# Performance work log

Hardware: AMD Instinct MI355X
Metric: run time of the kernel (lower is better)

The kernel has to match this reference:

```python
import jax, jax.numpy as jnp
import numpy as np

N = 50000      # nodes
E = 800000     # edges (avg degree 16)
F_IN = 128
H = 128


def setup_inputs() -> dict:
    key = jax.random.key(0)
    k = jax.random.split(key, 6)
    x = jax.random.normal(k[0], (N, F_IN), dtype=jnp.float32)
    edge_index = jax.random.randint(k[1], (2, E), 0, N, dtype=jnp.int64)
    perm = jax.random.permutation(k[2], N).astype(jnp.int64)
    # GCNConv params (PyG default: weight [F_in,H] applied as x @ W, bias [H])
    W = jax.random.normal(k[3], (F_IN, H), dtype=jnp.float32) / np.sqrt(F_IN)
    b = jnp.zeros((H,), dtype=jnp.float32)
    # nn.Bilinear(H, H, 1): weight [1,H,H], bias [1]
    bound = 1.0 / np.sqrt(H)
    Wb = jax.random.uniform(k[4], (1, H, H), dtype=jnp.float32, minval=-bound, maxval=bound)
    bb = jax.random.uniform(k[5], (1,), dtype=jnp.float32, minval=-bound, maxval=bound)
    return {"x": x, "W": W, "b": b, "Wb": Wb, "bb": bb,
            "edge_index": edge_index, "perm": perm}


def _gcn_conv(x, W, b, edge_index):
    # GCNConv: D^{-1/2} (A + I) D^{-1/2} X W + b  (symmetric norm, self-loops)
    xw = x @ W                               # [N, H] dense transform first
    loops = jnp.arange(N, dtype=edge_index.dtype)
    src = jnp.concatenate([edge_index[0], loops])   # [E+N]
    dst = jnp.concatenate([edge_index[1], loops])
    deg = jax.ops.segment_sum(jnp.ones_like(dst, dtype=xw.dtype), dst,
                              num_segments=N)        # in-degree incl. self-loop
    dinv = jnp.where(deg > 0, jax.lax.rsqrt(deg), 0.0)
    coef = dinv[src] * dinv[dst]                     # [E+N]
    msg = xw[src] * coef[:, None]                    # gather + scale
    z = jax.ops.segment_sum(msg, dst, num_segments=N) + b
    return z


def _bilinear(z1, z2, Wb, bb):
    # nn.Bilinear with out_features=1: score_n = z1_n^T Wb[0] z2_n + bb
    return jnp.einsum('nh,hg,ng->n', z1, Wb[0], z2)[:, None] + bb


def reference(x, W, b, Wb, bb, edge_index, perm):
    z = _gcn_conv(x, W, b, edge_index)
    positive_score = _bilinear(z, z, Wb, bb)
    negative_score = _bilinear(z, z[perm], Wb, bb)
    return (positive_score, negative_score)
```

## Files before the change

kernel.cpp:

```cpp
#include <hip/hip_runtime.h>
#include <hip/hip_bf16.h>

#define NN 50000
#define NE 800000
#define HD 128
#define WPAD 136

#define BINSH 9
#define NBINS 98
#define BINCAP 9216
#define CHUNK 1024
#define MAXBIN 9216

#define GEMM_BLOCKS ((NN + 63) / 64)
#define BIN_BLOCKS  ((NE + CHUNK - 1) / CHUNK)

typedef __attribute__((ext_vector_type(8))) short bf16x8;
typedef __attribute__((ext_vector_type(4))) float f32x4;

__device__ inline unsigned short f2bf(float f) {
    union { float f; unsigned u; } c; c.f = f;
    unsigned r = c.u + 0x7fff + ((c.u >> 16) & 1);
    return (unsigned short)(r >> 16);
}

__device__ inline float bflo(unsigned u) { return __uint_as_float(u << 16); }
__device__ inline float b2f(unsigned short u) { return __uint_as_float(((unsigned)u) << 16); }
__device__ inline float bfhi(unsigned u) { return __uint_as_float(u & 0xffff0000u); }

__device__ inline void split2(float v, unsigned short* h, unsigned short* l) {
    unsigned short hh = f2bf(v);
    float fh = __uint_as_float(((unsigned)hh) << 16);
    *h = hh;
    *l = f2bf(v - fh);
}

__device__ inline float4 ld_bf4(const unsigned short* p) {
    uint2 q = *(const uint2*)p;
    float4 r;
    r.x = bflo(q.x); r.y = bfhi(q.x);
    r.z = bflo(q.y); r.w = bfhi(q.y);
    return r;
}

__global__ __launch_bounds__(256) void k_prep(
        const float* __restrict__ W, const float* __restrict__ Wb, int* cursor,
        unsigned short* __restrict__ Wtg,
        unsigned short* __restrict__ Wbth, unsigned short* __restrict__ Wbtl) {
    int t = threadIdx.x;
    if (blockIdx.x == 0 && t < NBINS) cursor[t] = t * BINCAP;
    int idx = blockIdx.x * 256 + t;
    if (idx < HD * HD) {
        int h = idx >> 7, c = idx & 127;
        Wtg[c * WPAD + h] = f2bf(W[idx]);
        unsigned short hh, ll; split2(Wb[idx], &hh, &ll);
        Wbth[c * WPAD + h] = hh;
        Wbtl[c * WPAD + h] = ll;
    }
}

__global__ __launch_bounds__(256) void k_fused1(
        const float* __restrict__ x, const unsigned short* __restrict__ Wtg,
        unsigned short* __restrict__ ybf,
        const int* __restrict__ ei, int* cursor, unsigned* __restrict__ binned) {
    __shared__ union {
        unsigned short Wt[HD * WPAD];
        struct {
            unsigned stage[CHUNK];
            unsigned char sbin[CHUNK];
            int hist[NBINS], base[NBINS], cur[NBINS], gbase[NBINS];
        } p;
    } sh;
    int t = threadIdx.x;

    if (blockIdx.x < GEMM_BLOCKS) {
        int rowBase = blockIdx.x * 64;
        const uint4* src = (const uint4*)Wtg;
        uint4* dst = (uint4*)sh.Wt;
        #pragma unroll
        for (int i = 0; i < 9; ++i) {
            int f = t + i * 256;
            if (f < (HD * WPAD * 2) / 16) dst[f] = src[f];
        }
        __syncthreads();

        int w = t >> 6, lane = t & 63;
        int row = rowBase + w * 16 + (lane & 15);
        int rowc = row < NN ? row : NN - 1;
        int kbase = (lane >> 4) * 8;

        bf16x8 ah[4], al[4];
        const float* xrow = &x[(size_t)rowc * HD];
        #pragma unroll
        for (int kk = 0; kk < 4; ++kk) {
            float4 u0 = *(const float4*)(xrow + kk * 32 + kbase);
            float4 u1 = *(const float4*)(xrow + kk * 32 + kbase + 4);
            float vv[8] = {u0.x, u0.y, u0.z, u0.w, u1.x, u1.y, u1.z, u1.w};
            #pragma unroll
            for (int j = 0; j < 8; ++j) {
                unsigned short hh, ll; split2(vv[j], &hh, &ll);
                ah[kk][j] = (short)hh; al[kk][j] = (short)ll;
            }
        }

        f32x4 acc[8];
        #pragma unroll
        for (int ct = 0; ct < 8; ++ct) acc[ct] = (f32x4){0.f, 0.f, 0.f, 0.f};
        #pragma unroll
        for (int kk = 0; kk < 4; ++kk) {
            #pragma unroll
            for (int ct = 0; ct < 8; ++ct) {
                bf16x8 bfr = *(const bf16x8*)&sh.Wt[(ct * 16 + (lane & 15)) * WPAD + kk * 32 + kbase];
                acc[ct] = __builtin_amdgcn_mfma_f32_16x16x32_bf16(ah[kk], bfr, acc[ct], 0, 0, 0);
                acc[ct] = __builtin_amdgcn_mfma_f32_16x16x32_bf16(al[kk], bfr, acc[ct], 0, 0, 0);
            }
        }

        int r0 = rowBase + w * 16 + ((lane >> 4) << 2);
        #pragma unroll
        for (int r = 0; r < 4; ++r) {
            int gr = r0 + r;
            if (gr >= NN) continue;
            size_t basei = (size_t)gr * HD;
            #pragma unroll
            for (int ct = 0; ct < 8; ++ct)
                ybf[basei + ct * 16 + (lane & 15)] = f2bf(acc[ct][r]);
        }
    } else {
        int e0 = (blockIdx.x - GEMM_BLOCKS) * CHUNK;
        int nE = NE - e0; if (nE > CHUNK) nE = CHUNK;

        if (t < NBINS) sh.p.hist[t] = 0;
        __syncthreads();

        unsigned keys[CHUNK / 256], packs[CHUNK / 256];
        #pragma unroll
        for (int i = 0; i < CHUNK / 256; ++i) {
            int li = i * 256 + t;
            keys[i] = 0xffffffffu;
            if (li < nE) {
                int e = e0 + li;
                unsigned s = (unsigned)ei[e];
                unsigned d = (unsigned)ei[NE + e];
                if (s < NN && d < NN) {
                    keys[i] = d >> BINSH;
                    packs[i] = (s << BINSH) | (d & ((1u << BINSH) - 1));
                    atomicAdd(&sh.p.hist[keys[i]], 1);
                }
            }
        }
        __syncthreads();
        if (t == 0) { int a = 0; for (int b = 0; b < NBINS; ++b) { sh.p.base[b] = a; a += sh.p.hist[b]; } }
        __syncthreads();
        if (t < NBINS) {
            sh.p.cur[t] = sh.p.base[t];
            if (sh.p.hist[t] > 0) sh.p.gbase[t] = atomicAdd(&cursor[t], sh.p.hist[t]);
        }
        __syncthreads();
        #pragma unroll
        for (int i = 0; i < CHUNK / 256; ++i) {
            if (keys[i] != 0xffffffffu) {
                int p = atomicAdd(&sh.p.cur[keys[i]], 1);
                sh.p.stage[p] = packs[i];
                sh.p.sbin[p] = (unsigned char)keys[i];
            }
        }
        __syncthreads();
        int tot = sh.p.cur[NBINS - 1];
        for (int j = t; j < tot; j += 256) {
            unsigned b = sh.p.sbin[j];
            binned[sh.p.gbase[b] + (j - sh.p.base[b])] = sh.p.stage[j];
        }
    }
}

__global__ __launch_bounds__(256) void k_csr(
        const unsigned* __restrict__ binned, const int* __restrict__ cursor,
        unsigned short* __restrict__ csr, int* __restrict__ rowstart,
        int* __restrict__ degi, float* __restrict__ dinv) {
    __shared__ unsigned ent[MAXBIN];
    __shared__ unsigned short outv[MAXBIN];
    __shared__ int hist[512], rs[512], cur[512];
    __shared__ int sizes[NBINS];
    int t = threadIdx.x, b = blockIdx.x;

    if (t < NBINS) sizes[t] = cursor[t] - t * BINCAP;
    __syncthreads();
    int bsize = sizes[b]; if (bsize > MAXBIN) bsize = MAXBIN;
    int bstart = 0;
    for (int i = 0; i < b; ++i) bstart += sizes[i];

    for (int j = t; j < bsize; j += 256) ent[j] = binned[b * BINCAP + j];
    for (int k = t; k < 512; k += 256) hist[k] = 0;
    __syncthreads();
    for (int j = t; j < bsize; j += 256) atomicAdd(&hist[ent[j] & 511], 1);
    __syncthreads();
    if (t == 0) { int a = 0; for (int k = 0; k < 512; ++k) { rs[k] = a; a += hist[k]; } }
    __syncthreads();
    for (int k = t; k < 512; k += 256) {
        cur[k] = rs[k];
        int g = (b << BINSH) + k;
        if (g < NN) {
            rowstart[g] = bstart + rs[k];
            degi[g] = hist[k];
            dinv[g] = rsqrtf((float)(hist[k] + 1));
        }
    }
    __syncthreads();
    for (int j = t; j < bsize; j += 256) {
        unsigned v = ent[j];
        int p = atomicAdd(&cur[v & 511], 1);
        outv[p] = (unsigned short)(v >> BINSH);
    }
    __syncthreads();
    for (int j = t; j < bsize; j += 256) csr[bstart + j] = outv[j];
}

__global__ __launch_bounds__(256) void k_gather(
        const unsigned short* __restrict__ csr, const int* __restrict__ rowstart,
        const int* __restrict__ degi, const float* __restrict__ dinv,
        const unsigned short* __restrict__ ybf, const float* __restrict__ b,
        unsigned short* __restrict__ zbf) {
    int t = threadIdx.x;
    int n = blockIdx.x * 8 + (t >> 5);
    int lane = t & 31;
    if (n >= NN) return;
    int c = lane * 4;

    float dvn = dinv[n];
    float4 self = ld_bf4(&ybf[(size_t)n * HD + c]);
    float4 acc;
    acc.x = self.x * dvn; acc.y = self.y * dvn;
    acc.z = self.z * dvn; acc.w = self.w * dvn;
    int beg = rowstart[n];
    int dg = degi[n];

    int i = 0;
    for (; i + 8 <= dg; i += 8) {
        int ss[8];
        #pragma unroll
        for (int u = 0; u < 8; ++u) ss[u] = csr[beg + i + u];
        float dd[8];
        float4 vv[8];
        #pragma unroll
        for (int u = 0; u < 8; ++u) {
            dd[u] = dinv[ss[u]];
            vv[u] = ld_bf4(&ybf[(size_t)ss[u] * HD + c]);
        }
        #pragma unroll
        for (int u = 0; u < 8; ++u) {
            acc.x += vv[u].x * dd[u];
            acc.y += vv[u].y * dd[u];
            acc.z += vv[u].z * dd[u];
            acc.w += vv[u].w * dd[u];
        }
    }
    for (; i < dg; ++i) {
        int s = csr[beg + i];
        float ds = dinv[s];
        float4 v = ld_bf4(&ybf[(size_t)s * HD + c]);
        acc.x += v.x * ds; acc.y += v.y * ds;
        acc.z += v.z * ds; acc.w += v.w * ds;
    }

    float4 bv = *(const float4*)&b[c];
    ushort4 o;
    o.x = f2bf(acc.x * dvn + bv.x);
    o.y = f2bf(acc.y * dvn + bv.y);
    o.z = f2bf(acc.z * dvn + bv.z);
    o.w = f2bf(acc.w * dvn + bv.w);
    *(ushort4*)&zbf[(size_t)n * HD + c] = o;
}

__global__ __launch_bounds__(256) void k_bilinear(
        const unsigned short* __restrict__ zbf,
        const unsigned short* __restrict__ Wbth, const unsigned short* __restrict__ Wbtl,
        const float* __restrict__ bb, const int* __restrict__ perm,
        float* __restrict__ out) {
    __shared__ unsigned short Wth[HD * WPAD];
    __shared__ unsigned short Wtl[HD * WPAD];
    int t = threadIdx.x;
    int rowBase = blockIdx.x * 64;

    {
        const uint4* sh = (const uint4*)Wbth;
        const uint4* sl = (const uint4*)Wbtl;
        uint4* dh = (uint4*)Wth;
        uint4* dl = (uint4*)Wtl;
        #pragma unroll
        for (int i = 0; i < 9; ++i) {
            int f = t + i * 256;
            if (f < (HD * WPAD * 2) / 16) { dh[f] = sh[f]; dl[f] = sl[f]; }
        }
    }
    __syncthreads();

    int w = t >> 6, lane = t & 63;
    int row = rowBase + w * 16 + (lane & 15);
    int rowc = row < NN ? row : NN - 1;
    int kbase = (lane >> 4) * 8;

    bf16x8 za[4];
    const unsigned short* zrow = &zbf[(size_t)rowc * HD];
    #pragma unroll
    for (int kk = 0; kk < 4; ++kk)
        za[kk] = *(const bf16x8*)&zrow[kk * 32 + kbase];

    f32x4 acc[8];
    #pragma unroll
    for (int ct = 0; ct < 8; ++ct) acc[ct] = (f32x4){0.f, 0.f, 0.f, 0.f};
    #pragma unroll
    for (int kk = 0; kk < 4; ++kk) {
        #pragma unroll
        for (int ct = 0; ct < 8; ++ct) {
            int o = (ct * 16 + (lane & 15)) * WPAD + kk * 32 + kbase;
            bf16x8 bh = *(const bf16x8*)&Wth[o];
            bf16x8 bl = *(const bf16x8*)&Wtl[o];
            acc[ct] = __builtin_amdgcn_mfma_f32_16x16x32_bf16(za[kk], bh, acc[ct], 0, 0, 0);
            acc[ct] = __builtin_amdgcn_mfma_f32_16x16x32_bf16(za[kk], bl, acc[ct], 0, 0, 0);
        }
    }

    float bbv = bb[0];
    int r0 = rowBase + w * 16 + ((lane >> 4) << 2);
    float pos[4] = {0.f, 0.f, 0.f, 0.f}, neg[4] = {0.f, 0.f, 0.f, 0.f};
    #pragma unroll
    for (int r = 0; r < 4; ++r) {
        int gr = (r0 + r < NN) ? r0 + r : NN - 1;
        int pr = perm[gr];
        const unsigned short* zr = &zbf[(size_t)gr * HD];
        const unsigned short* zp = &zbf[(size_t)pr * HD];
        #pragma unroll
        for (int ct = 0; ct < 8; ++ct) {
            float tv = acc[ct][r];
            int col = ct * 16 + (lane & 15);
            pos[r] += tv * b2f(zr[col]);
            neg[r] += tv * b2f(zp[col]);
        }
    }
    #pragma unroll
    for (int r = 0; r < 4; ++r) {
        #pragma unroll
        for (int off = 1; off < 16; off <<= 1) {
            pos[r] += __shfl_xor(pos[r], off);
            neg[r] += __shfl_xor(neg[r], off);
        }
    }
    if ((lane & 15) == 0) {
        #pragma unroll
        for (int r = 0; r < 4; ++r) {
            int gr = r0 + r;
            if (gr < NN) {
                out[gr] = pos[r] + bbv;
                out[NN + gr] = neg[r] + bbv;
            }
        }
    }
}

extern "C" void kernel_launch(void* const* d_in, const int* in_sizes, int n_in,
                              void* d_out, int out_size, void* d_ws, size_t ws_size,
                              hipStream_t stream) {
    const float* x    = (const float*)d_in[0];
    const float* W    = (const float*)d_in[1];
    const float* b    = (const float*)d_in[2];
    const float* Wb   = (const float*)d_in[3];
    const float* bb   = (const float*)d_in[4];
    const int*   ei   = (const int*)d_in[5];
    const int*   perm = (const int*)d_in[6];
    float* out = (float*)d_out;

    char* ws = (char*)d_ws;
    int*            cursor   = (int*)(ws + 0);
    float*          dinv     = (float*)(ws + 0x1000);
    int*            rowstart = (int*)(ws + 0x33000);
    int*            degi     = (int*)(ws + 0x65000);
    unsigned short* csr      = (unsigned short*)(ws + 0x97000);
    unsigned*       binned   = (unsigned*)(ws + 0x240000);
    unsigned short* Wtg      = (unsigned short*)(ws + 0x5B0000);
    unsigned short* Wbth     = (unsigned short*)(ws + 0x5C0000);
    unsigned short* Wbtl     = (unsigned short*)(ws + 0x5D0000);
    unsigned short* ybf      = (unsigned short*)(ws + 0x600000);
    unsigned short* zbf      = (unsigned short*)(ws + 0x2000000);

    k_prep<<<(HD * HD + 255) / 256, 256, 0, stream>>>(W, Wb, cursor, Wtg, Wbth, Wbtl);
    k_fused1<<<GEMM_BLOCKS + BIN_BLOCKS, 256, 0, stream>>>(x, Wtg, ybf, ei, cursor, binned);
    k_csr<<<NBINS, 256, 0, stream>>>(binned, cursor, csr, rowstart, degi, dinv);
    k_gather<<<(NN + 7) / 8, 256, 0, stream>>>(csr, rowstart, degi, dinv, ybf, b, zbf);
    k_bilinear<<<GEMM_BLOCKS, 256, 0, stream>>>(zbf, Wbth, Wbtl, bb, perm, out);
}
```

Baseline: 95.06 us.

## Drop split-bf16 compensation, widen gather vectors, enlarge CSR blocks

Removes the hi/lo bf16 split for x and Wb, so each GEMM runs a single MFMA per tile instead of two and half the weight staging traffic goes away. The gather kernel now uses 16 lanes per node with 16-byte loads of 8 bf16 values instead of 32 lanes with 8-byte loads. The CSR build kernel moves to 512 threads per block. The cost is lower precision in both the dense transform and the bilinear score, which risks tolerance failures.

```diff
diff --git a/kernel.cpp b/kernel.cpp
--- a/kernel.cpp
+++ b/kernel.cpp
@@ -25,37 +25,19 @@
 }
 
 __device__ inline float bflo(unsigned u) { return __uint_as_float(u << 16); }
+__device__ inline float bfhi(unsigned u) { return __uint_as_float(u & 0xffff0000u); }
 __device__ inline float b2f(unsigned short u) { return __uint_as_float(((unsigned)u) << 16); }
-__device__ inline float bfhi(unsigned u) { return __uint_as_float(u & 0xffff0000u); }
-
-__device__ inline void split2(float v, unsigned short* h, unsigned short* l) {
-    unsigned short hh = f2bf(v);
-    float fh = __uint_as_float(((unsigned)hh) << 16);
-    *h = hh;
-    *l = f2bf(v - fh);
-}
-
-__device__ inline float4 ld_bf4(const unsigned short* p) {
-    uint2 q = *(const uint2*)p;
-    float4 r;
-    r.x = bflo(q.x); r.y = bfhi(q.x);
-    r.z = bflo(q.y); r.w = bfhi(q.y);
-    return r;
-}
 
 __global__ __launch_bounds__(256) void k_prep(
         const float* __restrict__ W, const float* __restrict__ Wb, int* cursor,
-        unsigned short* __restrict__ Wtg,
-        unsigned short* __restrict__ Wbth, unsigned short* __restrict__ Wbtl) {
+        unsigned short* __restrict__ Wtg, unsigned short* __restrict__ Wbth) {
     int t = threadIdx.x;
     if (blockIdx.x == 0 && t < NBINS) cursor[t] = t * BINCAP;
     int idx = blockIdx.x * 256 + t;
     if (idx < HD * HD) {
         int h = idx >> 7, c = idx & 127;
         Wtg[c * WPAD + h] = f2bf(W[idx]);
-        unsigned short hh, ll; split2(Wb[idx], &hh, &ll);
-        Wbth[c * WPAD + h] = hh;
-        Wbtl[c * WPAD + h] = ll;
+        Wbth[c * WPAD + h] = f2bf(Wb[idx]);
     }
 }
 
@@ -89,18 +71,16 @@
         int rowc = row < NN ? row : NN - 1;
         int kbase = (lane >> 4) * 8;
 
-        bf16x8 ah[4], al[4];
+        bf16x8 ah[4];
         const float* xrow = &x[(size_t)rowc * HD];
         #pragma unroll
         for (int kk = 0; kk < 4; ++kk) {
             float4 u0 = *(const float4*)(xrow + kk * 32 + kbase);
             float4 u1 = *(const float4*)(xrow + kk * 32 + kbase + 4);
-            float vv[8] = {u0.x, u0.y, u0.z, u0.w, u1.x, u1.y, u1.z, u1.w};
-            #pragma unroll
-            for (int j = 0; j < 8; ++j) {
-                unsigned short hh, ll; split2(vv[j], &hh, &ll);
-                ah[kk][j] = (short)hh; al[kk][j] = (short)ll;
-            }
+            ah[kk][0] = (short)f2bf(u0.x); ah[kk][1] = (short)f2bf(u0.y);
+            ah[kk][2] = (short)f2bf(u0.z); ah[kk][3] = (short)f2bf(u0.w);
+            ah[kk][4] = (short)f2bf(u1.x); ah[kk][5] = (short)f2bf(u1.y);
+            ah[kk][6] = (short)f2bf(u1.z); ah[kk][7] = (short)f2bf(u1.w);
         }
 
         f32x4 acc[8];
@@ -112,7 +92,6 @@
             for (int ct = 0; ct < 8; ++ct) {
                 bf16x8 bfr = *(const bf16x8*)&sh.Wt[(ct * 16 + (lane & 15)) * WPAD + kk * 32 + kbase];
                 acc[ct] = __builtin_amdgcn_mfma_f32_16x16x32_bf16(ah[kk], bfr, acc[ct], 0, 0, 0);
-                acc[ct] = __builtin_amdgcn_mfma_f32_16x16x32_bf16(al[kk], bfr, acc[ct], 0, 0, 0);
             }
         }
 
@@ -174,7 +153,7 @@
     }
 }
 
-__global__ __launch_bounds__(256) void k_csr(
+__global__ __launch_bounds__(512) void k_csr(
         const unsigned* __restrict__ binned, const int* __restrict__ cursor,
         unsigned short* __restrict__ csr, int* __restrict__ rowstart,
         int* __restrict__ degi, float* __restrict__ dinv) {
@@ -190,30 +169,30 @@
     int bstart = 0;
     for (int i = 0; i < b; ++i) bstart += sizes[i];
 
-    for (int j = t; j < bsize; j += 256) ent[j] = binned[b * BINCAP + j];
-    for (int k = t; k < 512; k += 256) hist[k] = 0;
-    __syncthreads();
-    for (int j = t; j < bsize; j += 256) atomicAdd(&hist[ent[j] & 511], 1);
+    for (int j = t; j < bsize; j += 512) ent[j] = binned[b * BINCAP + j];
+    if (t < 512) hist[t] = 0;
+    __syncthreads();
+    for (int j = t; j < bsize; j += 512) atomicAdd(&hist[ent[j] & 511], 1);
     __syncthreads();
     if (t == 0) { int a = 0; for (int k = 0; k < 512; ++k) { rs[k] = a; a += hist[k]; } }
     __syncthreads();
-    for (int k = t; k < 512; k += 256) {
-        cur[k] = rs[k];
-        int g = (b << BINSH) + k;
+    if (t < 512) {
+        cur[t] = rs[t];
+        int g = (b << BINSH) + t;
         if (g < NN) {
-            rowstart[g] = bstart + rs[k];
-            degi[g] = hist[k];
-            dinv[g] = rsqrtf((float)(hist[k] + 1));
-        }
-    }
-    __syncthreads();
-    for (int j = t; j < bsize; j += 256) {
+            rowstart[g] = bstart + rs[t];
+            degi[g] = hist[t];
+            dinv[g] = rsqrtf((float)(hist[t] + 1));
+        }
+    }
+    __syncthreads();
+    for (int j = t; j < bsize; j += 512) {
         unsigned v = ent[j];
         int p = atomicAdd(&cur[v & 511], 1);
         outv[p] = (unsigned short)(v >> BINSH);
     }
     __syncthreads();
-    for (int j = t; j < bsize; j += 256) csr[bstart + j] = outv[j];
+    for (int j = t; j < bsize; j += 512) csr[bstart + j] = outv[j];
 }
 
 __global__ __launch_bounds__(256) void k_gather(
@@ -222,16 +201,20 @@
         const unsigned short* __restrict__ ybf, const float* __restrict__ b,
         unsigned short* __restrict__ zbf) {
     int t = threadIdx.x;
-    int n = blockIdx.x * 8 + (t >> 5);
-    int lane = t & 31;
+    int n = blockIdx.x * 16 + (t >> 4);
+    int lane = t & 15;
     if (n >= NN) return;
-    int c = lane * 4;
+    int c = lane * 8;
 
     float dvn = dinv[n];
-    float4 self = ld_bf4(&ybf[(size_t)n * HD + c]);
-    float4 acc;
-    acc.x = self.x * dvn; acc.y = self.y * dvn;
-    acc.z = self.z * dvn; acc.w = self.w * dvn;
+    float acc[8];
+    {
+        uint4 q = *(const uint4*)&ybf[(size_t)n * HD + c];
+        acc[0] = bflo(q.x) * dvn; acc[1] = bfhi(q.x) * dvn;
+        acc[2] = bflo(q.y) * dvn; acc[3] = bfhi(q.y) * dvn;
+        acc[4] = bflo(q.z) * dvn; acc[5] = bfhi(q.z) * dvn;
+        acc[6] = bflo(q.w) * dvn; acc[7] = bfhi(q.w) * dvn;
+    }
     int beg = rowstart[n];
     int dg = degi[n];
 
@@ -241,56 +224,56 @@
         #pragma unroll
         for (int u = 0; u < 8; ++u) ss[u] = csr[beg + i + u];
         float dd[8];
-        float4 vv[8];
+        uint4 q[8];
         #pragma unroll
         for (int u = 0; u < 8; ++u) {
             dd[u] = dinv[ss[u]];
-            vv[u] = ld_bf4(&ybf[(size_t)ss[u] * HD + c]);
+            q[u] = *(const uint4*)&ybf[(size_t)ss[u] * HD + c];
         }
         #pragma unroll
         for (int u = 0; u < 8; ++u) {
-            acc.x += vv[u].x * dd[u];
-            acc.y += vv[u].y * dd[u];
-            acc.z += vv[u].z * dd[u];
-            acc.w += vv[u].w * dd[u];
+            acc[0] += bflo(q[u].x) * dd[u]; acc[1] += bfhi(q[u].x) * dd[u];
+            acc[2] += bflo(q[u].y) * dd[u]; acc[3] += bfhi(q[u].y) * dd[u];
+            acc[4] += bflo(q[u].z) * dd[u]; acc[5] += bfhi(q[u].z) * dd[u];
+            acc[6] += bflo(q[u].w) * dd[u]; acc[7] += bfhi(q[u].w) * dd[u];
         }
     }
     for (; i < dg; ++i) {
         int s = csr[beg + i];
         float ds = dinv[s];
-        float4 v = ld_bf4(&ybf[(size_t)s * HD + c]);
-        acc.x += v.x * ds; acc.y += v.y * ds;
-        acc.z += v.z * ds; acc.w += v.w * ds;
-    }
-
-    float4 bv = *(const float4*)&b[c];
-    ushort4 o;
-    o.x = f2bf(acc.x * dvn + bv.x);
-    o.y = f2bf(acc.y * dvn + bv.y);
-    o.z = f2bf(acc.z * dvn + bv.z);
-    o.w = f2bf(acc.w * dvn + bv.w);
-    *(ushort4*)&zbf[(size_t)n * HD + c] = o;
+        uint4 q = *(const uint4*)&ybf[(size_t)s * HD + c];
+        acc[0] += bflo(q.x) * ds; acc[1] += bfhi(q.x) * ds;
+        acc[2] += bflo(q.y) * ds; acc[3] += bfhi(q.y) * ds;
+        acc[4] += bflo(q.z) * ds; acc[5] += bfhi(q.z) * ds;
+        acc[6] += bflo(q.w) * ds; acc[7] += bfhi(q.w) * ds;
+    }
+
+    float4 bv0 = *(const float4*)&b[c];
+    float4 bv1 = *(const float4*)&b[c + 4];
+    unsigned o0 = (unsigned)f2bf(acc[0] * dvn + bv0.x) | ((unsigned)f2bf(acc[1] * dvn + bv0.y) << 16);
+    unsigned o1 = (unsigned)f2bf(acc[2] * dvn + bv0.z) | ((unsigned)f2bf(acc[3] * dvn + bv0.w) << 16);
+    unsigned o2 = (unsigned)f2bf(acc[4] * dvn + bv1.x) | ((unsigned)f2bf(acc[5] * dvn + bv1.y) << 16);
+    unsigned o3 = (unsigned)f2bf(acc[6] * dvn + bv1.z) | ((unsigned)f2bf(acc[7] * dvn + bv1.w) << 16);
+    uint4 o = make_uint4(o0, o1, o2, o3);
+    *(uint4*)&zbf[(size_t)n * HD + c] = o;
 }
 
 __global__ __launch_bounds__(256) void k_bilinear(
         const unsigned short* __restrict__ zbf,
-        const unsigned short* __restrict__ Wbth, const unsigned short* __restrict__ Wbtl,
+        const unsigned short* __restrict__ Wbth,
         const float* __restrict__ bb, const int* __restrict__ perm,
         float* __restrict__ out) {
     __shared__ unsigned short Wth[HD * WPAD];
-    __shared__ unsigned short Wtl[HD * WPAD];
     int t = threadIdx.x;
     int rowBase = blockIdx.x * 64;
 
     {
-        const uint4* sh = (const uint4*)Wbth;
-        const uint4* sl = (const uint4*)Wbtl;
+        const uint4* shp = (const uint4*)Wbth;
         uint4* dh = (uint4*)Wth;
-        uint4* dl = (uint4*)Wtl;
         #pragma unroll
         for (int i = 0; i < 9; ++i) {
             int f = t + i * 256;
-            if (f < (HD * WPAD * 2) / 16) { dh[f] = sh[f]; dl[f] = sl[f]; }
+            if (f < (HD * WPAD * 2) / 16) dh[f] = shp[f];
         }
     }
     __syncthreads();
@@ -313,11 +296,8 @@
     for (int kk = 0; kk < 4; ++kk) {
         #pragma unroll
         for (int ct = 0; ct < 8; ++ct) {
-            int o = (ct * 16 + (lane & 15)) * WPAD + kk * 32 + kbase;
-            bf16x8 bh = *(const bf16x8*)&Wth[o];
-            bf16x8 bl = *(const bf16x8*)&Wtl[o];
+            bf16x8 bh = *(const bf16x8*)&Wth[(ct * 16 + (lane & 15)) * WPAD + kk * 32 + kbase];
             acc[ct] = __builtin_amdgcn_mfma_f32_16x16x32_bf16(za[kk], bh, acc[ct], 0, 0, 0);
-            acc[ct] = __builtin_amdgcn_mfma_f32_16x16x32_bf16(za[kk], bl, acc[ct], 0, 0, 0);
         }
     }
 
@@ -379,13 +359,12 @@
     unsigned*       binned   = (unsigned*)(ws + 0x240000);
     unsigned short* Wtg      = (unsigned short*)(ws + 0x5B0000);
     unsigned short* Wbth     = (unsigned short*)(ws + 0x5C0000);
-    unsigned short* Wbtl     = (unsigned short*)(ws + 0x5D0000);
     unsigned short* ybf      = (unsigned short*)(ws + 0x600000);
     unsigned short* zbf      = (unsigned short*)(ws + 0x2000000);
 
-    k_prep<<<(HD * HD + 255) / 256, 256, 0, stream>>>(W, Wb, cursor, Wtg, Wbth, Wbtl);
+    k_prep<<<(HD * HD + 255) / 256, 256, 0, stream>>>(W, Wb, cursor, Wtg, Wbth);
     k_fused1<<<GEMM_BLOCKS + BIN_BLOCKS, 256, 0, stream>>>(x, Wtg, ybf, ei, cursor, binned);
-    k_csr<<<NBINS, 256, 0, stream>>>(binned, cursor, csr, rowstart, degi, dinv);
-    k_gather<<<(NN + 7) / 8, 256, 0, stream>>>(csr, rowstart, degi, dinv, ybf, b, zbf);
-    k_bilinear<<<GEMM_BLOCKS, 256, 0, stream>>>(zbf, Wbth, Wbtl, bb, perm, out);
-}
+    k_csr<<<NBINS, 512, 0, stream>>>(binned, cursor, csr, rowstart, degi, dinv);
+    k_gather<<<(NN + 15) / 16, 256, 0, stream>>>(csr, rowstart, degi, dinv, ybf, b, zbf);
+    k_bilinear<<<GEMM_BLOCKS, 256, 0, stream>>>(zbf, Wbth, bb, perm, out);
+}
```

Result: no change. 93.94 us (-1.2%).
